# Kernel tuning notes

Hardware: AMD Instinct MI355X
Metric: run time of the kernel (lower is better)

Reference implementation:

```python
import jax, jax.numpy as jnp
import numpy as np

B, L, HID, LOW = 1024, 64, 512, 20
TEMP = 1.0
EPS = 1e-20


def setup_inputs() -> dict:
    key = jax.random.key(0)
    ks = jax.random.split(key, 8)
    input_h = jax.random.normal(ks[0], (B, L, HID), jnp.float32)
    input_c = jax.random.normal(ks[1], (B, L, HID), jnp.float32)
    length = jax.random.randint(ks[2], (B,), L // 2, L + 1)          # valid lengths in [L/2, L]
    u_noise = jax.random.uniform(ks[3], (L - 1, B, L - 1), jnp.float32)  # gumbel uniforms per level
    s = 1.0 / np.sqrt(HID)
    W_reduce = jax.random.uniform(ks[4], (HID, LOW), jnp.float32, -s, s)
    b_reduce = jnp.zeros((LOW,), jnp.float32)
    s2 = 1.0 / np.sqrt(2 * LOW)
    W_comp = jax.random.uniform(ks[5], (2 * LOW, 5 * LOW), jnp.float32, -s2, s2)
    b_comp = jnp.zeros((5 * LOW,), jnp.float32)
    query = jax.random.normal(ks[6], (LOW,), jnp.float32) / np.sqrt(LOW)
    return dict(input_h=input_h, input_c=input_c, W_reduce=W_reduce, b_reduce=b_reduce,
                W_comp=W_comp, b_comp=b_comp, query=query, u_noise=u_noise, length=length)


def _treelstm(hl, cl, hr, cr, W, b):
    # BinaryTreeLSTMLayer.forward: concat children, one Linear to 5 gates
    v = jnp.concatenate([hl, hr], axis=-1) @ W + b          # (B, n, 5*LOW)
    i_, fl, fr, u_, o = jnp.split(v, 5, axis=-1)
    c = cl * jax.nn.sigmoid(fl + 1.0) + cr * jax.nn.sigmoid(fr + 1.0) \
        + jnp.tanh(u_) * jax.nn.sigmoid(i_)
    h = jax.nn.sigmoid(o) * jnp.tanh(c)
    return h, c


def _masked_softmax(logits, mask):
    probs = jax.nn.softmax(logits, axis=1)
    probs = probs * mask + EPS
    return probs / probs.sum(axis=1, keepdims=True)


def _st_gumbel(logits, u, mask):
    g = -jnp.log(-jnp.log(u + EPS) + EPS)                   # gumbel noise (non-diff, matches .data)
    y = _masked_softmax((logits + g) / TEMP, mask)
    y_hard = jax.nn.one_hot(jnp.argmax(y, axis=1), y.shape[1], dtype=y.dtype)
    return jax.lax.stop_gradient(y_hard - y) + y            # straight-through


def _forward(input_h, input_c, W_reduce, b_reduce, W_comp, b_comp, query, u_noise, length):
    h = input_h @ W_reduce + b_reduce                       # (B, L, LOW)  reduce_dim
    c = input_c @ W_reduce + b_reduce
    length_mask = (jnp.arange(L)[None, :] < length[:, None]).astype(h.dtype)  # (B, L)
    for i in range(L - 1):                                  # sequential DP over pyramid levels
        hl, cl = h[:, :-1], c[:, :-1]
        hr, cr = h[:, 1:], c[:, 1:]
        nh, nc = _treelstm(hl, cl, hr, cr, W_comp, b_comp)  # (B, L-1-i, LOW) all adjacent merges
        if i < L - 2:
            logits = nh @ query                             # dot_nd scoring, (B, L-1-i)
            sel = _st_gumbel(logits, u_noise[i, :, :L - 1 - i], length_mask[:, i + 1:])
            cum = jnp.cumsum(sel, axis=1)
            left = (1.0 - cum)[..., None]                   # keep old left spans
            right = (cum - sel)[..., None]                  # shift old right spans
            se = sel[..., None]
            nh = se * nh + left * hl + right * hr
            nc = se * nc + left * cl + right * cr
        done = length_mask[:, i + 1][:, None, None]         # update_state done_mask
        h = done * nh + (1.0 - done) * hl
        c = done * nc + (1.0 - done) * cl
    return h[:, 0]                                          # (B, LOW) root hidden state


def reference(input_h, input_c, W_reduce, b_reduce, W_comp, b_comp, query, u_noise, length):
    return _forward(input_h, input_c, W_reduce, b_reduce, W_comp, b_comp, query, u_noise, length)
```

## Files before the change

kernel.cpp:

```cpp
#include <hip/hip_runtime.h>
#include <cmath>
#include <cfloat>

namespace {

constexpr int kB   = 1024;
constexpr int kL   = 64;
constexpr int kHid = 512;
constexpr int kLow = 20;
constexpr int kLM1 = 63;
constexpr int kRowElems = kL * kLow;

__device__ __forceinline__ float fsig(float x) {
  return __builtin_amdgcn_rcpf(1.0f + __expf(-x));
}
__device__ __forceinline__ float ftanhf(float x) {
  return 1.0f - 2.0f * __builtin_amdgcn_rcpf(1.0f + __expf(2.0f * x));
}
__device__ __forceinline__ int rdl_i(int v, int l) {
  return __builtin_amdgcn_readlane(v, l);
}
__device__ __forceinline__ float rdl_f(float v, int l) {
  return __int_as_float(__builtin_amdgcn_readlane(__float_as_int(v), l));
}

#define DPPI(v, ctrl) __builtin_amdgcn_update_dpp((v), (v), (ctrl), 0xF, 0xF, false)
#define DPPF(v, ctrl) __int_as_float(DPPI(__float_as_int(v), (ctrl)))
#define DPPF0(v, ctrl)                                                        \
  __int_as_float(__builtin_amdgcn_update_dpp(0, __float_as_int(v), (ctrl),    \
                                             0xF, 0xF, true))

#define AMAX_STAGE(CTRL)                                                      \
  {                                                                           \
    const float oz = DPPF(zz, CTRL);                                          \
    const int   oi = DPPI(ji, CTRL);                                          \
    if (oz > zz || (oz == zz && oi < ji)) { zz = oz; ji = oi; }               \
  }

__global__ __launch_bounds__(256, 3)
void reduce_kernel(const float* __restrict__ Xh, const float* __restrict__ Xc,
                   const float* __restrict__ W, const float* __restrict__ bv,
                   float* __restrict__ H0, float* __restrict__ C0) {
  __shared__ float xs[64 * 132];
  __shared__ float wsm[128 * 20];

  const int bid = blockIdx.x;
  const float* __restrict__ X = (bid < kB) ? Xh : Xc;
  float* __restrict__ O       = (bid < kB) ? H0 : C0;
  const int b = bid & (kB - 1);
  X += (size_t)b * kL * kHid;
  O += (size_t)b * kRowElems;

  const int tid  = threadIdx.x;
  const int wave = tid >> 6;
  const int lane = tid & 63;

  float acc[20];
#pragma unroll
  for (int d = 0; d < 20; ++d) acc[d] = 0.0f;

  for (int ch = 0; ch < 4; ++ch) {
    __syncthreads();
#pragma unroll
    for (int r = 0; r < 8; ++r) {
      int f   = r * 256 + tid;
      int row = f >> 5;
      int c4  = (f & 31) << 2;
      float4 v = *(const float4*)(X + row * kHid + ch * 128 + c4);
      *(float4*)(xs + row * 132 + c4) = v;
    }
#pragma unroll
    for (int r = 0; r < 10; ++r) {
      int f = r * 256 + tid;
      wsm[f] = W[ch * 2560 + f];
    }
    __syncthreads();
#pragma unroll
    for (int kk = 0; kk < 32; ++kk) {
      int k = wave * 32 + kk;
      float x = xs[lane * 132 + k];
      const float4* wp = (const float4*)(wsm + k * 20);
      float4 w0 = wp[0], w1 = wp[1], w2 = wp[2], w3 = wp[3], w4 = wp[4];
      acc[0]  = fmaf(x, w0.x, acc[0]);  acc[1]  = fmaf(x, w0.y, acc[1]);
      acc[2]  = fmaf(x, w0.z, acc[2]);  acc[3]  = fmaf(x, w0.w, acc[3]);
      acc[4]  = fmaf(x, w1.x, acc[4]);  acc[5]  = fmaf(x, w1.y, acc[5]);
      acc[6]  = fmaf(x, w1.z, acc[6]);  acc[7]  = fmaf(x, w1.w, acc[7]);
      acc[8]  = fmaf(x, w2.x, acc[8]);  acc[9]  = fmaf(x, w2.y, acc[9]);
      acc[10] = fmaf(x, w2.z, acc[10]); acc[11] = fmaf(x, w2.w, acc[11]);
      acc[12] = fmaf(x, w3.x, acc[12]); acc[13] = fmaf(x, w3.y, acc[13]);
      acc[14] = fmaf(x, w3.z, acc[14]); acc[15] = fmaf(x, w3.w, acc[15]);
      acc[16] = fmaf(x, w4.x, acc[16]); acc[17] = fmaf(x, w4.y, acc[17]);
      acc[18] = fmaf(x, w4.z, acc[18]); acc[19] = fmaf(x, w4.w, acc[19]);
    }
  }

  __syncthreads();
  float* red = xs;
#pragma unroll
  for (int d = 0; d < 20; ++d) red[wave * 1280 + lane * 20 + d] = acc[d];
  __syncthreads();
#pragma unroll
  for (int r = 0; r < 5; ++r) {
    int f = r * 256 + tid;
    float s = (red[f] + red[1280 + f]) + (red[2560 + f] + red[3840 + f]);
    O[f] = s + bv[f % 20];
  }
}

#define EVAL_UNIT(A_, B2_, PS_, DD_, HN_)                                     \
  {                                                                           \
    float ai = bcs[DD_], af = bcs[20 + DD_], ag = bcs[40 + DD_],              \
          au = bcs[60 + DD_], ao = bcs[80 + DD_];                             \
    const int xa_ = (A_)*20, xb_ = (B2_)*20, wr_ = (DD_)*44;                  \
    _Pragma("unroll")                                                         \
    for (int kq = 0; kq < 10; ++kq) {                                         \
      const float4 xq = (kq < 5)                                              \
          ? *(const float4*)(h_state + xa_ + kq * 4)                          \
          : *(const float4*)(h_state + xb_ + (kq - 5) * 4);                   \
      const float4 wi = *(const float4*)(Wt + wr_ + kq * 4);                  \
      const float4 wf = *(const float4*)(Wt + 880  + wr_ + kq * 4);           \
      const float4 wg = *(const float4*)(Wt + 1760 + wr_ + kq * 4);           \
      const float4 wu = *(const float4*)(Wt + 2640 + wr_ + kq * 4);           \
      const float4 wo = *(const float4*)(Wt + 3520 + wr_ + kq * 4);           \
      ai = fmaf(xq.x, wi.x, ai); ai = fmaf(xq.y, wi.y, ai);                   \
      ai = fmaf(xq.z, wi.z, ai); ai = fmaf(xq.w, wi.w, ai);                   \
      af = fmaf(xq.x, wf.x, af); af = fmaf(xq.y, wf.y, af);                   \
      af = fmaf(xq.z, wf.z, af); af = fmaf(xq.w, wf.w, af);                   \
      ag = fmaf(xq.x, wg.x, ag); ag = fmaf(xq.y, wg.y, ag);                   \
      ag = fmaf(xq.z, wg.z, ag); ag = fmaf(xq.w, wg.w, ag);                   \
      au = fmaf(xq.x, wu.x, au); au = fmaf(xq.y, wu.y, au);                   \
      au = fmaf(xq.z, wu.z, au); au = fmaf(xq.w, wu.w, au);                   \
      ao = fmaf(xq.x, wo.x, ao); ao = fmaf(xq.y, wo.y, ao);                   \
      ao = fmaf(xq.z, wo.z, ao); ao = fmaf(xq.w, wo.w, ao);                   \
    }                                                                         \
    const float cl_ = c_state[(A_)*20 + (DD_)],                               \
                cr_ = c_state[(B2_)*20 + (DD_)];                              \
    const float cn_ = cl_ * fsig(af + 1.0f) + cr_ * fsig(ag + 1.0f) +         \
                      ftanhf(au) * fsig(ai);                                  \
    (HN_) = fsig(ao) * ftanhf(cn_);                                           \
    nh[(PS_)*20 + (DD_)] = (HN_);                                             \
    nc[(PS_)*20 + (DD_)] = cn_;                                               \
  }

#define EVAL_REGW(PHA_, PHB_, PCA_, PCB_, PS_)                                \
  {                                                                           \
    float xr[40];                                                             \
    _Pragma("unroll")                                                         \
    for (int q = 0; q < 5; ++q) {                                             \
      const float4 t = *(const float4*)((PHA_) + q * 4);                      \
      xr[q*4+0]=t.x; xr[q*4+1]=t.y; xr[q*4+2]=t.z; xr[q*4+3]=t.w;             \
    }                                                                         \
    _Pragma("unroll")                                                         \
    for (int q = 0; q < 5; ++q) {                                             \
      const float4 t = *(const float4*)((PHB_) + q * 4);                      \
      xr[20+q*4+0]=t.x; xr[20+q*4+1]=t.y; xr[20+q*4+2]=t.z; xr[20+q*4+3]=t.w; \
    }                                                                         \
    float si = bi, sfl = bfl, sfr = bfr, su = bu, so = bo;                    \
    _Pragma("unroll")                                                         \
    for (int kk = 0; kk < 40; ++kk) {                                         \
      si  = fmaf(xr[kk], w0[kk], si);                                         \
      sfl = fmaf(xr[kk], w1[kk], sfl);                                        \
      sfr = fmaf(xr[kk], w2[kk], sfr);                                        \
      su  = fmaf(xr[kk], w3[kk], su);                                         \
      so  = fmaf(xr[kk], w4[kk], so);                                         \
    }                                                                         \
    const float cl_ = (PCA_)[dd];                                             \
    const float cr_ = (PCB_)[dd];                                             \
    const float cn_ = cl_ * fsig(sfl + 1.0f) + cr_ * fsig(sfr + 1.0f) +       \
                      ftanhf(su) * fsig(si);                                  \
    const float hn_ = fsig(so) * ftanhf(cn_);                                 \
    nh[(PS_)*20 + dd] = hn_;                                                  \
    nc[(PS_)*20 + dd] = cn_;                                                  \
    part_ = hn_ * qq;                                                         \
  }

__global__ __launch_bounds__(64, 1)
void pyramid_kernel(const float* __restrict__ H0, const float* __restrict__ C0,
                    const float* __restrict__ Wc, const float* __restrict__ bcg,
                    const float* __restrict__ query, const float* __restrict__ U,
                    const int* __restrict__ length, float* __restrict__ out) {
  __shared__ float h_state[64 * 20];
  __shared__ float c_state[64 * 20];
  __shared__ float nh[63 * 20];
  __shared__ float nc[63 * 20];
  __shared__ float Wt[100 * 44];
  __shared__ float bcs[100];
  __shared__ float qvs[20];

  const int b    = blockIdx.x;
  const int lane = threadIdx.x;
  const int dd   = lane & 31;
  const int ddc  = dd < 20 ? dd : 19;
  int len = length[b];
  len = len < 1 ? 1 : (len > 64 ? 64 : len);

  {
    const float4* h4 = (const float4*)(H0 + (size_t)b * kRowElems);
    const float4* c4 = (const float4*)(C0 + (size_t)b * kRowElems);
#pragma unroll
    for (int r = 0; r < 5; ++r) {
      int f = r * 64 + lane;
      ((float4*)h_state)[f] = h4[f];
      ((float4*)c_state)[f] = c4[f];
    }
  }
  for (int f = lane; f < 4000; f += 64) {
    int c = f / 40, k = f - c * 40;
    Wt[c * 44 + k] = Wc[k * 100 + c];
  }
  for (int f = lane; f < 100; f += 64) bcs[f] = bcg[f];
  if (lane < 20) qvs[lane] = query[lane];

  int   idx_r  = lane;
  int   pidx_r = lane;
  float lgt_r  = -FLT_MAX;

  const int col = lane < 62 ? lane : 62;
  const float u_row0 = U[b * kLM1 + col];
  float u_c = (kLM1 > 1) ? U[1 * (kB * kLM1) + b * kLM1 + col] : 0.0f;

#pragma unroll 1
  for (int r = 0; r < 20; ++r) {
    int uu = r * 64 + lane;
    if (uu < 1260) {
      int p = uu / 20, d2 = uu - p * 20;
      float hn_;
      EVAL_UNIT(p, p + 1, p, d2, hn_);
      (void)hn_;
    }
  }
  if (lane < 63) {
    float s = 0.0f;
#pragma unroll
    for (int q = 0; q < 5; ++q) {
      const float4 t  = *(const float4*)(nh  + lane * 20 + q * 4);
      const float4 qv = *(const float4*)(qvs + q * 4);
      s = fmaf(t.x, qv.x, s); s = fmaf(t.y, qv.y, s);
      s = fmaf(t.z, qv.z, s); s = fmaf(t.w, qv.w, s);
    }
    lgt_r = s;
  }

  float w0[40], w1[40], w2[40], w3[40], w4[40];
#pragma unroll
  for (int q = 0; q < 10; ++q) {
    float4 t;
    t = *(const float4*)(Wt + (0  + ddc) * 44 + q * 4);
    w0[q*4+0]=t.x; w0[q*4+1]=t.y; w0[q*4+2]=t.z; w0[q*4+3]=t.w;
    t = *(const float4*)(Wt + (20 + ddc) * 44 + q * 4);
    w1[q*4+0]=t.x; w1[q*4+1]=t.y; w1[q*4+2]=t.z; w1[q*4+3]=t.w;
    t = *(const float4*)(Wt + (40 + ddc) * 44 + q * 4);
    w2[q*4+0]=t.x; w2[q*4+1]=t.y; w2[q*4+2]=t.z; w2[q*4+3]=t.w;
    t = *(const float4*)(Wt + (60 + ddc) * 44 + q * 4);
    w3[q*4+0]=t.x; w3[q*4+1]=t.y; w3[q*4+2]=t.z; w3[q*4+3]=t.w;
    t = *(const float4*)(Wt + (80 + ddc) * 44 + q * 4);
    w4[q*4+0]=t.x; w4[q*4+1]=t.y; w4[q*4+2]=t.z; w4[q*4+3]=t.w;
  }
#pragma unroll
  for (int j = 0; j < 40; ++j) {
    asm volatile("" : "+v"(w0[j]), "+v"(w1[j]), "+v"(w2[j]),
                      "+v"(w3[j]), "+v"(w4[j]));
  }
  const float bi  = bcs[ddc],      bfl = bcs[20 + ddc], bfr = bcs[40 + ddc],
              bu  = bcs[60 + ddc], bo  = bcs[80 + ddc];
  const float qq  = qvs[ddc];

  float gcur = -__logf(-__logf(u_row0 + 1e-20f) + 1e-20f);

  const int nIter = len - 1;
#pragma unroll 1
  for (int i = 0; i < nIter; ++i) {
    const int n = kL - i;

    float zz = -FLT_MAX;
    int   ji = lane;
    if ((lane <= n - 2) && ((i + 1 + lane) < len)) zz = lgt_r + gcur;
    AMAX_STAGE(0xB1);
    AMAX_STAGE(0x4E);
    AMAX_STAGE(0x141);
    AMAX_STAGE(0x140);
    AMAX_STAGE(0x142);
    AMAX_STAGE(0x143);
    const int k = rdl_i(ji, 63);

    float u_d = 0.0f;
    if (i + 2 <= kLM1 - 1) u_d = U[(i + 2) * (kB * kLM1) + b * kLM1 + col];

    const int km1 = (k >= 1) ? k - 1 : 0;
    const int kp2 = (k <= n - 3) ? k + 2 : 0;
    const int tgt = rdl_i(idx_r,  k);
    const int psk = rdl_i(pidx_r, k);
    const int iA  = rdl_i(idx_r,  km1);
    const int pA  = rdl_i(pidx_r, km1);
    const int iB  = rdl_i(idx_r,  kp2);

    if (lane < 20) {
      h_state[tgt * 20 + lane] = nh[psk * 20 + lane];
      c_state[tgt * 20 + lane] = nc[psk * 20 + lane];
    }

    {
      int   sI = DPPI(idx_r,  0x101);
      int   sP = DPPI(pidx_r, 0x101);
      float sL = DPPF(lgt_r,  0x101);
      const int   bi16 = rdl_i(idx_r, 16),  bi32 = rdl_i(idx_r, 32),
                  bi48 = rdl_i(idx_r, 48);
      const int   bp16 = rdl_i(pidx_r, 16), bp32 = rdl_i(pidx_r, 32),
                  bp48 = rdl_i(pidx_r, 48);
      const float bl16 = rdl_f(lgt_r, 16),  bl32 = rdl_f(lgt_r, 32),
                  bl48 = rdl_f(lgt_r, 48);
      if (lane == 15) { sI = bi16; sP = bp16; sL = bl16; }
      if (lane == 31) { sI = bi32; sP = bp32; sL = bl32; }
      if (lane == 47) { sI = bi48; sP = bp48; sL = bl48; }
      const bool doI = (lane >= k + 1) && (lane <= n - 2);
      const bool doP = (lane >= k + 1) && (lane <= n - 3);
      if (doI) idx_r = sI;
      if (doP) { pidx_r = sP; lgt_r = sL; }
    }

    if (i < len - 2) {
      const int  p    = lane >> 5;
      const bool hasB = (k >= 1) && (k <= n - 3);
      const float *pHA, *pHB, *pCA, *pCB;
      int PS2;
      if (p == 0 && k >= 1) {
        pHA = h_state + iA * 20;  pCA = c_state + iA * 20;
        pHB = nh + psk * 20;      pCB = nc + psk * 20;
        PS2 = pA;
      } else {
        pHA = nh + psk * 20;      pCA = nc + psk * 20;
        pHB = h_state + iB * 20;  pCB = c_state + iB * 20;
        PS2 = psk;
      }
      const bool act = (dd < 20) && ((p == 0) || hasB);
      float part_ = 0.0f;
      if (act) { EVAL_REGW(pHA, pHB, pCA, pCB, PS2); }
      part_ += DPPF0(part_, 0xB1);
      part_ += DPPF0(part_, 0x4E);
      part_ += DPPF0(part_, 0x141);
      part_ += DPPF0(part_, 0x140);
      part_ += DPPF0(part_, 0x142);
      const float vA = rdl_f(part_, 31);
      const float vB = rdl_f(part_, 63);
      const int   pos0 = (k >= 1) ? k - 1 : k;
      if (lane == pos0) lgt_r = vA;
      if (hasB && lane == k) lgt_r = vB;
    }

    gcur = -__logf(-__logf(u_c + 1e-20f) + 1e-20f);
    u_c  = u_d;
  }

  const int root = rdl_i(idx_r, 0);
  if (lane < 20) {
    out[b * 20 + lane] = h_state[root * 20 + lane];
  }
}

}

extern "C" void kernel_launch(void* const* d_in, const int* in_sizes, int n_in,
                              void* d_out, int out_size, void* d_ws, size_t ws_size,
                              hipStream_t stream) {
  const float* input_h  = (const float*)d_in[0];
  const float* input_c  = (const float*)d_in[1];
  const float* W_reduce = (const float*)d_in[2];
  const float* b_reduce = (const float*)d_in[3];
  const float* W_comp   = (const float*)d_in[4];
  const float* b_comp   = (const float*)d_in[5];
  const float* query    = (const float*)d_in[6];
  const float* u_noise  = (const float*)d_in[7];
  const int*   length   = (const int*)d_in[8];
  float* out = (float*)d_out;

  float* H0 = (float*)d_ws;
  float* C0 = H0 + (size_t)kB * kL * kLow;

  reduce_kernel<<<dim3(2 * kB), dim3(256), 0, stream>>>(
      input_h, input_c, W_reduce, b_reduce, H0, C0);
  pyramid_kernel<<<dim3(kB), dim3(64), 0, stream>>>(
      H0, C0, W_comp, b_comp, query, u_noise, length, out);
}
```

Measured before the change: 174.7 us.

## Split gate dot-products across wave halves and use packed-key argmax with ballot

The per-step tree-LSTM evaluation now splits the 40-wide input dot product into two 20-wide halves, one per half-wave, and combines them with a cross-half shuffle. Both candidate merges (left and right of the selected position) are evaluated by all lanes. This halves the per-lane weight registers (100 instead of 200 floats) and the serial FMA chain length, at the cost of two evaluations, extra shuffles and duplicated transcendental work. The argmax reduction is also changed to a single-value unsigned max on order-preserving float keys, followed by a ballot and find-first-set to recover the lowest index, which replaces the paired float/index DPP exchanges.

New measurement: 174.9 us. Within noise of the previous version (+0.2%).

```diff
diff --git a/kernel.cpp b/kernel.cpp
--- a/kernel.cpp
+++ b/kernel.cpp
@@ -29,12 +29,10 @@
 #define DPPF0(v, ctrl)                                                        \
   __int_as_float(__builtin_amdgcn_update_dpp(0, __float_as_int(v), (ctrl),    \
                                              0xF, 0xF, true))
-
-#define AMAX_STAGE(CTRL)                                                      \
+#define UMAX_STAGE(CTRL)                                                      \
   {                                                                           \
-    const float oz = DPPF(zz, CTRL);                                          \
-    const int   oi = DPPI(ji, CTRL);                                          \
-    if (oz > zz || (oz == zz && oi < ji)) { zz = oz; ji = oi; }               \
+    const unsigned o_ = (unsigned)DPPI((int)m, CTRL);                         \
+    m = (m > o_) ? m : o_;                                                    \
   }
 
 __global__ __launch_bounds__(256, 3)
@@ -142,36 +140,35 @@
     nc[(PS_)*20 + (DD_)] = cn_;                                               \
   }
 
-#define EVAL_REGW(PHA_, PHB_, PCA_, PCB_, PS_)                                \
+#define EVAL_KS(PXA_, PXB_, PCL_, PCR_, HN_, CN_)                             \
   {                                                                           \
-    float xr[40];                                                             \
+    const float* xp_ = half ? (PXB_) : (PXA_);                                \
+    float xr_[20];                                                            \
     _Pragma("unroll")                                                         \
-    for (int q = 0; q < 5; ++q) {                                             \
-      const float4 t = *(const float4*)((PHA_) + q * 4);                      \
-      xr[q*4+0]=t.x; xr[q*4+1]=t.y; xr[q*4+2]=t.z; xr[q*4+3]=t.w;             \
+    for (int q_ = 0; q_ < 5; ++q_) {                                          \
+      const float4 t_ = *(const float4*)(xp_ + q_ * 4);                       \
+      xr_[q_*4+0]=t_.x; xr_[q_*4+1]=t_.y; xr_[q_*4+2]=t_.z; xr_[q_*4+3]=t_.w; \
     }                                                                         \
+    float si_=0.f, sfl_=0.f, sfr_=0.f, su_=0.f, so_=0.f;                      \
     _Pragma("unroll")                                                         \
-    for (int q = 0; q < 5; ++q) {                                             \
-      const float4 t = *(const float4*)((PHB_) + q * 4);                      \
-      xr[20+q*4+0]=t.x; xr[20+q*4+1]=t.y; xr[20+q*4+2]=t.z; xr[20+q*4+3]=t.w; \
+    for (int kk_ = 0; kk_ < 20; ++kk_) {                                      \
+      si_  = fmaf(xr_[kk_], w0[kk_], si_);                                    \
+      sfl_ = fmaf(xr_[kk_], w1[kk_], sfl_);                                   \
+      sfr_ = fmaf(xr_[kk_], w2[kk_], sfr_);                                   \
+      su_  = fmaf(xr_[kk_], w3[kk_], su_);                                    \
+      so_  = fmaf(xr_[kk_], w4[kk_], so_);                                    \
     }                                                                         \
-    float si = bi, sfl = bfl, sfr = bfr, su = bu, so = bo;                    \
-    _Pragma("unroll")                                                         \
-    for (int kk = 0; kk < 40; ++kk) {                                         \
-      si  = fmaf(xr[kk], w0[kk], si);                                         \
-      sfl = fmaf(xr[kk], w1[kk], sfl);                                        \
-      sfr = fmaf(xr[kk], w2[kk], sfr);                                        \
-      su  = fmaf(xr[kk], w3[kk], su);                                         \
-      so  = fmaf(xr[kk], w4[kk], so);                                         \
-    }                                                                         \
-    const float cl_ = (PCA_)[dd];                                             \
-    const float cr_ = (PCB_)[dd];                                             \
-    const float cn_ = cl_ * fsig(sfl + 1.0f) + cr_ * fsig(sfr + 1.0f) +       \
-                      ftanhf(su) * fsig(si);                                  \
-    const float hn_ = fsig(so) * ftanhf(cn_);                                 \
-    nh[(PS_)*20 + dd] = hn_;                                                  \
-    nc[(PS_)*20 + dd] = cn_;                                                  \
-    part_ = hn_ * qq;                                                         \
+    si_  += __shfl_xor(si_, 32);                                              \
+    sfl_ += __shfl_xor(sfl_, 32);                                             \
+    sfr_ += __shfl_xor(sfr_, 32);                                             \
+    su_  += __shfl_xor(su_, 32);                                              \
+    so_  += __shfl_xor(so_, 32);                                              \
+    si_ += bi; sfl_ += bfl; sfr_ += bfr; su_ += bu; so_ += bo;                \
+    const float cl_ = (PCL_)[ddc];                                            \
+    const float cr_ = (PCR_)[ddc];                                            \
+    (CN_) = cl_ * fsig(sfl_ + 1.0f) + cr_ * fsig(sfr_ + 1.0f) +               \
+            ftanhf(su_) * fsig(si_);                                          \
+    (HN_) = fsig(so_) * ftanhf(CN_);                                          \
   }
 
 __global__ __launch_bounds__(64, 1)
@@ -189,6 +186,7 @@
 
   const int b    = blockIdx.x;
   const int lane = threadIdx.x;
+  const int half = lane >> 5;
   const int dd   = lane & 31;
   const int ddc  = dd < 20 ? dd : 19;
   int len = length[b];
@@ -241,23 +239,23 @@
     lgt_r = s;
   }
 
-  float w0[40], w1[40], w2[40], w3[40], w4[40];
-#pragma unroll
-  for (int q = 0; q < 10; ++q) {
+  float w0[20], w1[20], w2[20], w3[20], w4[20];
+#pragma unroll
+  for (int q = 0; q < 5; ++q) {
     float4 t;
-    t = *(const float4*)(Wt + (0  + ddc) * 44 + q * 4);
+    t = *(const float4*)(Wt + (0  + ddc) * 44 + half * 20 + q * 4);
     w0[q*4+0]=t.x; w0[q*4+1]=t.y; w0[q*4+2]=t.z; w0[q*4+3]=t.w;
-    t = *(const float4*)(Wt + (20 + ddc) * 44 + q * 4);
+    t = *(const float4*)(Wt + (20 + ddc) * 44 + half * 20 + q * 4);
     w1[q*4+0]=t.x; w1[q*4+1]=t.y; w1[q*4+2]=t.z; w1[q*4+3]=t.w;
-    t = *(const float4*)(Wt + (40 + ddc) * 44 + q * 4);
+    t = *(const float4*)(Wt + (40 + ddc) * 44 + half * 20 + q * 4);
     w2[q*4+0]=t.x; w2[q*4+1]=t.y; w2[q*4+2]=t.z; w2[q*4+3]=t.w;
-    t = *(const float4*)(Wt + (60 + ddc) * 44 + q * 4);
+    t = *(const float4*)(Wt + (60 + ddc) * 44 + half * 20 + q * 4);
     w3[q*4+0]=t.x; w3[q*4+1]=t.y; w3[q*4+2]=t.z; w3[q*4+3]=t.w;
-    t = *(const float4*)(Wt + (80 + ddc) * 44 + q * 4);
+    t = *(const float4*)(Wt + (80 + ddc) * 44 + half * 20 + q * 4);
     w4[q*4+0]=t.x; w4[q*4+1]=t.y; w4[q*4+2]=t.z; w4[q*4+3]=t.w;
   }
 #pragma unroll
-  for (int j = 0; j < 40; ++j) {
+  for (int j = 0; j < 20; ++j) {
     asm volatile("" : "+v"(w0[j]), "+v"(w1[j]), "+v"(w2[j]),
                       "+v"(w3[j]), "+v"(w4[j]));
   }
@@ -272,16 +270,21 @@
   for (int i = 0; i < nIter; ++i) {
     const int n = kL - i;
 
-    float zz = -FLT_MAX;
-    int   ji = lane;
-    if ((lane <= n - 2) && ((i + 1 + lane) < len)) zz = lgt_r + gcur;
-    AMAX_STAGE(0xB1);
-    AMAX_STAGE(0x4E);
-    AMAX_STAGE(0x141);
-    AMAX_STAGE(0x140);
-    AMAX_STAGE(0x142);
-    AMAX_STAGE(0x143);
-    const int k = rdl_i(ji, 63);
+    const float zf = lgt_r + gcur;
+    const unsigned ub  = __float_as_uint(zf);
+    unsigned key = ((int)ub < 0) ? ~ub : (ub | 0x80000000u);
+    const bool valid = (lane <= n - 2) && ((i + 1 + lane) < len);
+    if (!valid) key = 0u;
+    unsigned m = key;
+    UMAX_STAGE(0xB1);
+    UMAX_STAGE(0x4E);
+    UMAX_STAGE(0x141);
+    UMAX_STAGE(0x140);
+    UMAX_STAGE(0x142);
+    UMAX_STAGE(0x143);
+    const unsigned gmax = (unsigned)rdl_i((int)m, 63);
+    const unsigned long long bal = __ballot(valid && (key == gmax));
+    const int k = (int)(__ffsll(bal) - 1);
 
     float u_d = 0.0f;
     if (i + 2 <= kLM1 - 1) u_d = U[(i + 2) * (kB * kLM1) + b * kLM1 + col];
@@ -319,32 +322,30 @@
     }
 
     if (i < len - 2) {
-      const int  p    = lane >> 5;
-      const bool hasB = (k >= 1) && (k <= n - 3);
-      const float *pHA, *pHB, *pCA, *pCB;
-      int PS2;
-      if (p == 0 && k >= 1) {
-        pHA = h_state + iA * 20;  pCA = c_state + iA * 20;
-        pHB = nh + psk * 20;      pCB = nc + psk * 20;
-        PS2 = pA;
-      } else {
-        pHA = nh + psk * 20;      pCA = nc + psk * 20;
-        pHB = h_state + iB * 20;  pCB = c_state + iB * 20;
-        PS2 = psk;
+      const bool hasA = (k >= 1);
+      const bool hasB = (k <= n - 3);
+      float hnA, cnA, hnB, cnB;
+      EVAL_KS(h_state + iA * 20, nh + psk * 20,
+              c_state + iA * 20, nc + psk * 20, hnA, cnA);
+      EVAL_KS(nh + psk * 20, h_state + iB * 20,
+              nc + psk * 20, c_state + iB * 20, hnB, cnB);
+      if (hasA && half == 0 && dd < 20) {
+        nh[pA * 20 + dd] = hnA;  nc[pA * 20 + dd] = cnA;
       }
-      const bool act = (dd < 20) && ((p == 0) || hasB);
-      float part_ = 0.0f;
-      if (act) { EVAL_REGW(pHA, pHB, pCA, pCB, PS2); }
-      part_ += DPPF0(part_, 0xB1);
-      part_ += DPPF0(part_, 0x4E);
-      part_ += DPPF0(part_, 0x141);
-      part_ += DPPF0(part_, 0x140);
-      part_ += DPPF0(part_, 0x142);
-      const float vA = rdl_f(part_, 31);
-      const float vB = rdl_f(part_, 63);
-      const int   pos0 = (k >= 1) ? k - 1 : k;
-      if (lane == pos0) lgt_r = vA;
-      if (hasB && lane == k) lgt_r = vB;
+      if (hasB && half == 1 && dd < 20) {
+        nh[psk * 20 + dd] = hnB; nc[psk * 20 + dd] = cnB;
+      }
+      float pr = 0.0f;
+      if (dd < 20) pr = half ? hnB * qq : hnA * qq;
+      pr += DPPF0(pr, 0xB1);
+      pr += DPPF0(pr, 0x4E);
+      pr += DPPF0(pr, 0x141);
+      pr += DPPF0(pr, 0x140);
+      pr += DPPF0(pr, 0x142);
+      const float vA = rdl_f(pr, 31);
+      const float vB = rdl_f(pr, 63);
+      if (hasA && lane == k - 1) lgt_r = vA;
+      if (hasB && lane == k)     lgt_r = vB;
     }
 
     gcur = -__logf(-__logf(u_c + 1e-20f) + 1e-20f);
```
